# Optimization experiments

Measured on AMD Instinct MI355X. Metric: run time of the kernel, lower is better.

The kernel has to match this reference:

```python
import jax, jax.numpy as jnp
import numpy as np

D = 4096  # input_dim
H = 4096  # hidden_dim


def setup_inputs() -> dict:
    key = jax.random.key(0)
    k_x, k_w, k_b, k_v, k_c = jax.random.split(key, 5)
    x = jax.random.uniform(k_x, (D, 1), dtype=jnp.float32)  # observed pixel values
    w = jax.random.normal(k_w, (H, D), dtype=jnp.float32) * 0.02
    b = jax.random.normal(k_b, (D, 1), dtype=jnp.float32) * 0.02
    v = jax.random.normal(k_v, (D, H), dtype=jnp.float32) * 0.02
    c = jax.random.normal(k_c, (H, 1), dtype=jnp.float32) * 0.02
    return {"x": x, "w": w, "b": b, "v": v, "c": c}


def reference(x, w, b, v, c):
    # Original loop: a_0 = c; a_{i+1} = a_i + w[:, i] * x[i]
    # => a_i = c + sum_{j < i} w[:, j] * x[j]  (exclusive cumsum of rank-1 updates)
    wx = w * x[:, 0][None, :]                      # [H, D]
    cum = jnp.cumsum(wx, axis=1)                   # inclusive cumsum over columns
    A = c + jnp.pad(cum[:, :-1], ((0, 0), (1, 0)))  # exclusive cumsum -> a_i in column i, [H, D]
    h = jax.nn.sigmoid(A)                          # h_i = sigmoid(a_i), [H, D]
    # p_i = sigmoid(v[i, :] @ h_i + b[i])
    logits = jnp.einsum("ih,hi->i", v, h)[:, None] + b  # [D, 1]
    p_x = jax.nn.sigmoid(logits)                   # [D, 1]
    return p_x
```

## Files before the change

kernel.cpp:

```cpp
#include <hip/hip_runtime.h>
#include <hip/hip_fp16.h>

#define D_DIM 4096
#define H_DIM 4096

__device__ __forceinline__ float fast_sigmoid(float a) {
    return __builtin_amdgcn_rcpf(1.0f + __expf(-a));
}

__global__ __launch_bounds__(256, 4) void nade_scan_kernel(
    const float* __restrict__ x,
    const float* __restrict__ w,
    const float* __restrict__ c,
    __half* __restrict__ S)
{
    const int tid  = threadIdx.x;
    const int lane = tid & 63;
    const int h    = blockIdx.x * 4 + (tid >> 6);

    const float* wrow = w + (size_t)h * D_DIM + 8 * lane;
    __half*      srow = S + (size_t)h * D_DIM + 8 * lane;
    float carry = c[h];

    float4 wc0 = *reinterpret_cast<const float4*>(wrow);
    float4 wc1 = *reinterpret_cast<const float4*>(wrow + 4);

    #pragma unroll
    for (int t = 0; t < 8; ++t) {
        float4 wn0, wn1;
        if (t < 7) {
            wn0 = *reinterpret_cast<const float4*>(wrow + (t + 1) * 512);
            wn1 = *reinterpret_cast<const float4*>(wrow + (t + 1) * 512 + 4);
        }
        float4 x0 = *reinterpret_cast<const float4*>(x + t * 512 + 8 * lane);
        float4 x1 = *reinterpret_cast<const float4*>(x + t * 512 + 8 * lane + 4);

        float p0 = wc0.x * x0.x, p1 = wc0.y * x0.y, p2 = wc0.z * x0.z, p3 = wc0.w * x0.w;
        float p4 = wc1.x * x1.x, p5 = wc1.y * x1.y, p6 = wc1.z * x1.z, p7 = wc1.w * x1.w;
        float s8 = ((p0 + p1) + (p2 + p3)) + ((p4 + p5) + (p6 + p7));
        float incl = s8;
        #pragma unroll
        for (int off = 1; off < 64; off <<= 1) {
            float tv = __shfl_up(incl, off, 64);
            incl += (lane >= off) ? tv : 0.0f;
        }
        float tot = __shfl(incl, 63, 64);
        float a = carry + incl - s8;
        float sg0 = fast_sigmoid(a); a += p0;
        float sg1 = fast_sigmoid(a); a += p1;
        float sg2 = fast_sigmoid(a); a += p2;
        float sg3 = fast_sigmoid(a); a += p3;
        float sg4 = fast_sigmoid(a); a += p4;
        float sg5 = fast_sigmoid(a); a += p5;
        float sg6 = fast_sigmoid(a); a += p6;
        float sg7 = fast_sigmoid(a);
        carry += tot;

        union { __half2 h2[4]; uint4 u; } P;
        P.h2[0] = __floats2half2_rn(sg0, sg1);
        P.h2[1] = __floats2half2_rn(sg2, sg3);
        P.h2[2] = __floats2half2_rn(sg4, sg5);
        P.h2[3] = __floats2half2_rn(sg6, sg7);
        *reinterpret_cast<uint4*>(srow + t * 512) = P.u;

        wc0 = wn0; wc1 = wn1;
    }
}

__global__ __launch_bounds__(256, 8) void nade_vdot_kernel(
    const float* __restrict__ v,
    const __half* __restrict__ S,
    float* __restrict__ part)
{
    __shared__ __half Sl[128][64];
    __shared__ float red[4][64];

    const int tid = threadIdx.x;
    const int it  = blockIdx.x & 63;
    const int ht  = blockIdx.x >> 6;
    const int i0  = it * 64;
    const int h0  = ht * 128;

    {
        const int r  = tid >> 3;
        const int c8 = tid & 7;
        #pragma unroll
        for (int p = 0; p < 4; ++p) {
            const int hh = p * 32 + r;
            uint4 d = *reinterpret_cast<const uint4*>(
                S + (size_t)(h0 + hh) * D_DIM + i0 + c8 * 8);
            *reinterpret_cast<uint4*>(&Sl[hh][c8 * 8]) = d;
        }
    }
    __syncthreads();

    const int il = tid & 63;
    const int q  = tid >> 6;
    const float* vp = v + (size_t)(i0 + il) * H_DIM + h0 + q * 32;

    float4 va[8];
    #pragma unroll
    for (int k = 0; k < 8; ++k)
        va[k] = *reinterpret_cast<const float4*>(vp + 4 * k);

    float acc = 0.0f;
    #pragma unroll
    for (int k = 0; k < 8; ++k) {
        const int hb = q * 32 + 4 * k;
        acc += va[k].x * __half2float(Sl[hb + 0][il])
             + va[k].y * __half2float(Sl[hb + 1][il])
             + va[k].z * __half2float(Sl[hb + 2][il])
             + va[k].w * __half2float(Sl[hb + 3][il]);
    }
    red[q][il] = acc;
    __syncthreads();
    if (q == 0)
        part[(size_t)ht * D_DIM + i0 + il] =
            red[0][il] + red[1][il] + red[2][il] + red[3][il];
}

__global__ __launch_bounds__(256, 8) void nade_out_kernel(
    const float* __restrict__ part,
    const float* __restrict__ b,
    float* __restrict__ out)
{
    const int i = blockIdx.x * 256 + threadIdx.x;
    float t = b[i];
    #pragma unroll
    for (int s = 0; s < 32; ++s)
        t += part[(size_t)s * D_DIM + i];
    out[i] = fast_sigmoid(t);
}

__global__ __launch_bounds__(1024, 1) void nade_fused_atomic(
    const float* __restrict__ x,
    const float* __restrict__ w,
    const float* __restrict__ v,
    const float* __restrict__ c,
    float* __restrict__ logits)
{
    __shared__ __half S[16][D_DIM];

    const int tid  = threadIdx.x;
    const int wv   = tid >> 6;
    const int lane = tid & 63;
    const int h0   = blockIdx.x * 16;

    const float* wrow = w + (size_t)(h0 + wv) * D_DIM + 8 * lane;
    float carry = c[h0 + wv];
    #pragma unroll
    for (int t = 0; t < 8; ++t) {
        float4 w0 = *reinterpret_cast<const float4*>(wrow + t * 512);
        float4 w1 = *reinterpret_cast<const float4*>(wrow + t * 512 + 4);
        float4 x0 = *reinterpret_cast<const float4*>(x + t * 512 + 8 * lane);
        float4 x1 = *reinterpret_cast<const float4*>(x + t * 512 + 8 * lane + 4);
        float p0 = w0.x * x0.x, p1 = w0.y * x0.y, p2 = w0.z * x0.z, p3 = w0.w * x0.w;
        float p4 = w1.x * x1.x, p5 = w1.y * x1.y, p6 = w1.z * x1.z, p7 = w1.w * x1.w;
        float s8 = ((p0 + p1) + (p2 + p3)) + ((p4 + p5) + (p6 + p7));
        float incl = s8;
        #pragma unroll
        for (int off = 1; off < 64; off <<= 1) {
            float tv = __shfl_up(incl, off, 64);
            incl += (lane >= off) ? tv : 0.0f;
        }
        float tot = __shfl(incl, 63, 64);
        float a = carry + incl - s8;
        float sg0 = fast_sigmoid(a); a += p0;
        float sg1 = fast_sigmoid(a); a += p1;
        float sg2 = fast_sigmoid(a); a += p2;
        float sg3 = fast_sigmoid(a); a += p3;
        float sg4 = fast_sigmoid(a); a += p4;
        float sg5 = fast_sigmoid(a); a += p5;
        float sg6 = fast_sigmoid(a); a += p6;
        float sg7 = fast_sigmoid(a);
        carry += tot;
        union { __half2 h2[4]; uint4 u; } P;
        P.h2[0] = __floats2half2_rn(sg0, sg1);
        P.h2[1] = __floats2half2_rn(sg2, sg3);
        P.h2[2] = __floats2half2_rn(sg4, sg5);
        P.h2[3] = __floats2half2_rn(sg6, sg7);
        *reinterpret_cast<uint4*>(&S[wv][t * 512 + 8 * lane]) = P.u;
    }
    __syncthreads();

    const int i0 = 4 * tid;
    float acc[4] = {0.f, 0.f, 0.f, 0.f};
    #pragma unroll
    for (int r = 0; r < 4; ++r) {
        const float* vp = v + (size_t)(i0 + r) * H_DIM + h0;
        float4 q0 = *reinterpret_cast<const float4*>(vp);
        float4 q1 = *reinterpret_cast<const float4*>(vp + 4);
        float4 q2 = *reinterpret_cast<const float4*>(vp + 8);
        float4 q3 = *reinterpret_cast<const float4*>(vp + 12);
        acc[r] = q0.x * __half2float(S[0][i0 + r])  + q0.y * __half2float(S[1][i0 + r])
               + q0.z * __half2float(S[2][i0 + r])  + q0.w * __half2float(S[3][i0 + r])
               + q1.x * __half2float(S[4][i0 + r])  + q1.y * __half2float(S[5][i0 + r])
               + q1.z * __half2float(S[6][i0 + r])  + q1.w * __half2float(S[7][i0 + r])
               + q2.x * __half2float(S[8][i0 + r])  + q2.y * __half2float(S[9][i0 + r])
               + q2.z * __half2float(S[10][i0 + r]) + q2.w * __half2float(S[11][i0 + r])
               + q3.x * __half2float(S[12][i0 + r]) + q3.y * __half2float(S[13][i0 + r])
               + q3.z * __half2float(S[14][i0 + r]) + q3.w * __half2float(S[15][i0 + r]);
    }
    #pragma unroll
    for (int r = 0; r < 4; ++r) atomicAdd(&logits[i0 + r], acc[r]);
}

__global__ __launch_bounds__(256, 1) void nade_final_atomic(
    const float* __restrict__ logits,
    const float* __restrict__ b,
    float* __restrict__ out)
{
    const int i = blockIdx.x * 256 + threadIdx.x;
    out[i] = fast_sigmoid(logits[i] + b[i]);
}

extern "C" void kernel_launch(void* const* d_in, const int* in_sizes, int n_in,
                              void* d_out, int out_size, void* d_ws, size_t ws_size,
                              hipStream_t stream)
{
    const float* x = (const float*)d_in[0];
    const float* w = (const float*)d_in[1];
    const float* b = (const float*)d_in[2];
    const float* v = (const float*)d_in[3];
    const float* c = (const float*)d_in[4];
    float* out = (float*)d_out;

    const size_t s_bytes    = (size_t)H_DIM * D_DIM * sizeof(__half);
    const size_t part_bytes = (size_t)32 * D_DIM * sizeof(float);

    if (ws_size >= s_bytes + part_bytes) {
        __half* S    = (__half*)d_ws;
        float*  part = (float*)((char*)d_ws + s_bytes);
        nade_scan_kernel<<<H_DIM / 4, 256, 0, stream>>>(x, w, c, S);
        nade_vdot_kernel<<<64 * 32, 256, 0, stream>>>(v, S, part);
        nade_out_kernel<<<D_DIM / 256, 256, 0, stream>>>(part, b, out);
    } else {
        float* logits = (float*)d_ws;
        hipMemsetAsync(logits, 0, D_DIM * sizeof(float), stream);
        nade_fused_atomic<<<H_DIM / 16, 1024, 0, stream>>>(x, w, v, c, logits);
        nade_final_atomic<<<D_DIM / 256, 256, 0, stream>>>(logits, b, out);
    }
}
```

Before: 45.73 us.

## Split scan rows across two wavefronts and pad shared tile in vdot kernel

The scan kernel now assigns two wavefronts per hidden row, each scanning half of the columns. Local prefix values are kept in registers, and the first half's total is passed to the second through shared memory before the sigmoid and store pass. This halves the serial chain per wave and raises parallelism, at the cost of a block barrier and 32 extra registers per thread. The vdot kernel's shared S tile row is padded from 64 to 80 halves, which appears aimed at reducing LDS bank conflicts.

```diff
diff --git a/kernel.cpp b/kernel.cpp
--- a/kernel.cpp
+++ b/kernel.cpp
@@ -3,38 +3,46 @@
 
 #define D_DIM 4096
 #define H_DIM 4096
+#define SLP 80
 
 __device__ __forceinline__ float fast_sigmoid(float a) {
     return __builtin_amdgcn_rcpf(1.0f + __expf(-a));
 }
 
-__global__ __launch_bounds__(256, 4) void nade_scan_kernel(
+__global__ __launch_bounds__(512, 6) void nade_scan_kernel(
     const float* __restrict__ x,
     const float* __restrict__ w,
     const float* __restrict__ c,
     __half* __restrict__ S)
 {
+    __shared__ float tot0[4];
+
     const int tid  = threadIdx.x;
+    const int wv   = tid >> 6;
     const int lane = tid & 63;
-    const int h    = blockIdx.x * 4 + (tid >> 6);
-
-    const float* wrow = w + (size_t)h * D_DIM + 8 * lane;
-    __half*      srow = S + (size_t)h * D_DIM + 8 * lane;
-    float carry = c[h];
+    const int rl   = wv >> 1;
+    const int half = wv & 1;
+    const int h    = blockIdx.x * 4 + rl;
+
+    const float* wrow = w + (size_t)h * D_DIM + half * 2048 + 8 * lane;
+    const float* xcol = x + half * 2048 + 8 * lane;
+    __half*      srow = S + (size_t)h * D_DIM + half * 2048 + 8 * lane;
+
+    float l[32];
+    float carry = 0.0f;
 
     float4 wc0 = *reinterpret_cast<const float4*>(wrow);
     float4 wc1 = *reinterpret_cast<const float4*>(wrow + 4);
 
     #pragma unroll
-    for (int t = 0; t < 8; ++t) {
+    for (int t = 0; t < 4; ++t) {
         float4 wn0, wn1;
-        if (t < 7) {
+        if (t < 3) {
             wn0 = *reinterpret_cast<const float4*>(wrow + (t + 1) * 512);
             wn1 = *reinterpret_cast<const float4*>(wrow + (t + 1) * 512 + 4);
         }
-        float4 x0 = *reinterpret_cast<const float4*>(x + t * 512 + 8 * lane);
-        float4 x1 = *reinterpret_cast<const float4*>(x + t * 512 + 8 * lane + 4);
-
+        float4 x0 = *reinterpret_cast<const float4*>(xcol + t * 512);
+        float4 x1 = *reinterpret_cast<const float4*>(xcol + t * 512 + 4);
         float p0 = wc0.x * x0.x, p1 = wc0.y * x0.y, p2 = wc0.z * x0.z, p3 = wc0.w * x0.w;
         float p4 = wc1.x * x1.x, p5 = wc1.y * x1.y, p6 = wc1.z * x1.z, p7 = wc1.w * x1.w;
         float s8 = ((p0 + p1) + (p2 + p3)) + ((p4 + p5) + (p6 + p7));
@@ -44,26 +52,32 @@
             float tv = __shfl_up(incl, off, 64);
             incl += (lane >= off) ? tv : 0.0f;
         }
-        float tot = __shfl(incl, 63, 64);
         float a = carry + incl - s8;
-        float sg0 = fast_sigmoid(a); a += p0;
-        float sg1 = fast_sigmoid(a); a += p1;
-        float sg2 = fast_sigmoid(a); a += p2;
-        float sg3 = fast_sigmoid(a); a += p3;
-        float sg4 = fast_sigmoid(a); a += p4;
-        float sg5 = fast_sigmoid(a); a += p5;
-        float sg6 = fast_sigmoid(a); a += p6;
-        float sg7 = fast_sigmoid(a);
-        carry += tot;
-
+        l[8*t+0] = a; a += p0;
+        l[8*t+1] = a; a += p1;
+        l[8*t+2] = a; a += p2;
+        l[8*t+3] = a; a += p3;
+        l[8*t+4] = a; a += p4;
+        l[8*t+5] = a; a += p5;
+        l[8*t+6] = a; a += p6;
+        l[8*t+7] = a;
+        carry += __shfl(incl, 63, 64);
+        wc0 = wn0; wc1 = wn1;
+    }
+
+    if (half == 0 && lane == 63) tot0[rl] = carry;
+    __syncthreads();
+
+    const float base = c[h] + (half ? tot0[rl] : 0.0f);
+
+    #pragma unroll
+    for (int t = 0; t < 4; ++t) {
         union { __half2 h2[4]; uint4 u; } P;
-        P.h2[0] = __floats2half2_rn(sg0, sg1);
-        P.h2[1] = __floats2half2_rn(sg2, sg3);
-        P.h2[2] = __floats2half2_rn(sg4, sg5);
-        P.h2[3] = __floats2half2_rn(sg6, sg7);
+        #pragma unroll
+        for (int j = 0; j < 4; ++j)
+            P.h2[j] = __floats2half2_rn(fast_sigmoid(l[8*t+2*j]   + base),
+                                        fast_sigmoid(l[8*t+2*j+1] + base));
         *reinterpret_cast<uint4*>(srow + t * 512) = P.u;
-
-        wc0 = wn0; wc1 = wn1;
     }
 }
 
@@ -72,7 +86,7 @@
     const __half* __restrict__ S,
     float* __restrict__ part)
 {
-    __shared__ __half Sl[128][64];
+    __shared__ __half Sl[128][SLP];
     __shared__ float red[4][64];
 
     const int tid = threadIdx.x;
@@ -231,7 +245,7 @@
     if (ws_size >= s_bytes + part_bytes) {
         __half* S    = (__half*)d_ws;
         float*  part = (float*)((char*)d_ws + s_bytes);
-        nade_scan_kernel<<<H_DIM / 4, 256, 0, stream>>>(x, w, c, S);
+        nade_scan_kernel<<<H_DIM / 4, 512, 0, stream>>>(x, w, c, S);
         nade_vdot_kernel<<<64 * 32, 256, 0, stream>>>(v, S, part);
         nade_out_kernel<<<D_DIM / 256, 256, 0, stream>>>(part, b, out);
     } else {
```

Measured after the change: 52.75 us. 15.4% more time.

## Deepen w prefetch to four tiles and pad shared S tile rows

Applied to the files above, without the earlier changes.

The scan kernel now keeps four tiles of w rows in flight in registers, rotating through four buffers, instead of prefetching only the next tile. It also prefetches x one tile ahead. The intent is to hide global load latency in this memory-bound scan. The vdot kernel's shared S tile row width is padded from 64 to 80 halves to reduce LDS bank conflicts, at the cost of more registers and shared memory, which may lower occupancy.

```diff
diff --git a/kernel.cpp b/kernel.cpp
--- a/kernel.cpp
+++ b/kernel.cpp
@@ -3,6 +3,7 @@
 
 #define D_DIM 4096
 #define H_DIM 4096
+#define SLP 80
 
 __device__ __forceinline__ float fast_sigmoid(float a) {
     return __builtin_amdgcn_rcpf(1.0f + __expf(-a));
@@ -22,21 +23,31 @@
     __half*      srow = S + (size_t)h * D_DIM + 8 * lane;
     float carry = c[h];
 
-    float4 wc0 = *reinterpret_cast<const float4*>(wrow);
-    float4 wc1 = *reinterpret_cast<const float4*>(wrow + 4);
-
-    #pragma unroll
-    for (int t = 0; t < 8; ++t) {
-        float4 wn0, wn1;
+    float4 wA0 = *reinterpret_cast<const float4*>(wrow + 0 * 512);
+    float4 wA1 = *reinterpret_cast<const float4*>(wrow + 0 * 512 + 4);
+    float4 wB0 = *reinterpret_cast<const float4*>(wrow + 1 * 512);
+    float4 wB1 = *reinterpret_cast<const float4*>(wrow + 1 * 512 + 4);
+    float4 wC0 = *reinterpret_cast<const float4*>(wrow + 2 * 512);
+    float4 wC1 = *reinterpret_cast<const float4*>(wrow + 2 * 512 + 4);
+    float4 wD0 = *reinterpret_cast<const float4*>(wrow + 3 * 512);
+    float4 wD1 = *reinterpret_cast<const float4*>(wrow + 3 * 512 + 4);
+
+    float4 xc0 = *reinterpret_cast<const float4*>(x + 8 * lane);
+    float4 xc1 = *reinterpret_cast<const float4*>(x + 8 * lane + 4);
+
+    auto tile = [&](int t, float4& WS0, float4& WS1) {
+        float4 u0 = WS0, u1 = WS1;
+        if (t + 4 < 8) {
+            WS0 = *reinterpret_cast<const float4*>(wrow + (t + 4) * 512);
+            WS1 = *reinterpret_cast<const float4*>(wrow + (t + 4) * 512 + 4);
+        }
+        float4 xn0, xn1;
         if (t < 7) {
-            wn0 = *reinterpret_cast<const float4*>(wrow + (t + 1) * 512);
-            wn1 = *reinterpret_cast<const float4*>(wrow + (t + 1) * 512 + 4);
-        }
-        float4 x0 = *reinterpret_cast<const float4*>(x + t * 512 + 8 * lane);
-        float4 x1 = *reinterpret_cast<const float4*>(x + t * 512 + 8 * lane + 4);
-
-        float p0 = wc0.x * x0.x, p1 = wc0.y * x0.y, p2 = wc0.z * x0.z, p3 = wc0.w * x0.w;
-        float p4 = wc1.x * x1.x, p5 = wc1.y * x1.y, p6 = wc1.z * x1.z, p7 = wc1.w * x1.w;
+            xn0 = *reinterpret_cast<const float4*>(x + (t + 1) * 512 + 8 * lane);
+            xn1 = *reinterpret_cast<const float4*>(x + (t + 1) * 512 + 8 * lane + 4);
+        }
+        float p0 = u0.x * xc0.x, p1 = u0.y * xc0.y, p2 = u0.z * xc0.z, p3 = u0.w * xc0.w;
+        float p4 = u1.x * xc1.x, p5 = u1.y * xc1.y, p6 = u1.z * xc1.z, p7 = u1.w * xc1.w;
         float s8 = ((p0 + p1) + (p2 + p3)) + ((p4 + p5) + (p6 + p7));
         float incl = s8;
         #pragma unroll
@@ -63,8 +74,11 @@
         P.h2[3] = __floats2half2_rn(sg6, sg7);
         *reinterpret_cast<uint4*>(srow + t * 512) = P.u;
 
-        wc0 = wn0; wc1 = wn1;
-    }
+        if (t < 7) { xc0 = xn0; xc1 = xn1; }
+    };
+
+    tile(0, wA0, wA1); tile(1, wB0, wB1); tile(2, wC0, wC1); tile(3, wD0, wD1);
+    tile(4, wA0, wA1); tile(5, wB0, wB1); tile(6, wC0, wC1); tile(7, wD0, wD1);
 }
 
 __global__ __launch_bounds__(256, 8) void nade_vdot_kernel(
@@ -72,7 +86,7 @@
     const __half* __restrict__ S,
     float* __restrict__ part)
 {
-    __shared__ __half Sl[128][64];
+    __shared__ __half Sl[128][SLP];
     __shared__ float red[4][64];
 
     const int tid = threadIdx.x;
```

Result: slower. 51.95 us (+13.6%).
